# Kernel tuning notes

Measured on AMD Instinct MI355X. Metric: run time of the kernel, lower is better.

## Reference

```python
import jax, jax.numpy as jnp
import numpy as np
from jax import lax

EPS = 1e-5

# sign binarization with straight-through estimator (bitorch Sign: grad clipped to |x|<=1)
def _sign(x):
    return jnp.where(x >= 0, 1.0, -1.0).astype(x.dtype)

@jax.custom_vjp
def sign_ste(x):
    return _sign(x)

def _sign_fwd(x):
    return _sign(x), x

def _sign_bwd(x, g):
    return (g * (jnp.abs(x) <= 1.0).astype(g.dtype),)

sign_ste.defvjp(_sign_fwd, _sign_bwd)


def conv2d(x, w, stride, padding):
    return lax.conv_general_dilated(
        x, w, window_strides=(stride, stride),
        padding=[(padding, padding), (padding, padding)],
        dimension_numbers=("NCHW", "OIHW", "NCHW"))


def batchnorm(x, gamma, beta, mean, var):
    # eval-mode BN with running statistics
    inv = gamma / jnp.sqrt(var + EPS)
    return x * inv[None, :, None, None] + (beta - mean * inv)[None, :, None, None]


def avgpool2(x, stride):
    # AvgPool2d(kernel_size=2, stride=stride); here stride==2, H,W even
    B, C, H, W = x.shape
    return x.reshape(B, C, H // 2, 2, W // 2, 2).mean(axis=(3, 5))


def setup_inputs() -> dict:
    key = jax.random.key(0)
    ks = jax.random.split(key, 6)
    B, Cin, Cout, H, W = 16, 32, 64, 224, 224
    x = jax.random.normal(ks[0], (B, Cin, H, W), dtype=jnp.float32)
    w_body = jax.random.normal(ks[1], (Cout, Cin, 3, 3), dtype=jnp.float32) * 0.1
    w_ds = jax.random.normal(ks[2], (Cout, Cin, 1, 1), dtype=jnp.float32) * 0.1
    bn1_gamma = jnp.ones((Cout,), jnp.float32)
    bn1_beta = jnp.zeros((Cout,), jnp.float32)
    bn1_mean = jax.random.normal(ks[3], (Cout,), dtype=jnp.float32) * 0.1
    bn1_var = jax.random.uniform(ks[4], (Cout,), dtype=jnp.float32) + 0.5
    bn2_gamma = jnp.ones((Cout,), jnp.float32)
    bn2_beta = jnp.zeros((Cout,), jnp.float32)
    bn2_mean = jax.random.normal(ks[5], (Cout,), dtype=jnp.float32) * 0.1
    bn2_var = jax.random.uniform(jax.random.fold_in(key, 7), (Cout,), dtype=jnp.float32) + 0.5
    return dict(x=x, w_body=w_body, bn1_gamma=bn1_gamma, bn1_beta=bn1_beta,
                bn1_mean=bn1_mean, bn1_var=bn1_var, w_ds=w_ds,
                bn2_gamma=bn2_gamma, bn2_beta=bn2_beta,
                bn2_mean=bn2_mean, bn2_var=bn2_var)


def reference(x, w_body, bn1_gamma, bn1_beta, bn1_mean, bn1_var,
              w_ds, bn2_gamma, bn2_beta, bn2_mean, bn2_var):
    stride = 2
    # downsample branch (full precision): AvgPool2d(2, stride) -> 1x1 conv -> BN
    residual = avgpool2(x, stride)
    residual = conv2d(residual, w_ds, stride=1, padding=0)
    residual = batchnorm(residual, bn2_gamma, bn2_beta, bn2_mean, bn2_var)
    # body: QConv2d with sign-quantized input and weight, then BN
    xb = sign_ste(x)
    wb = sign_ste(w_body)
    body = conv2d(xb, wb, stride=stride, padding=1)
    body = batchnorm(body, bn1_gamma, bn1_beta, bn1_mean, bn1_var)
    return body + residual
```

## Files before the change

kernel.cpp:

```cpp
#include <hip/hip_runtime.h>
#include <stdint.h>

static constexpr int NB = 16;
static constexpr int CI = 32;
static constexpr int CO = 64;
static constexpr int HI = 224, WI = 224;
static constexpr int HO = 112, WO = 112;
static constexpr int HW = HI * WI;
static constexpr float EPS = 1e-5f;

typedef _Float16 h2 __attribute__((ext_vector_type(2)));

__device__ __forceinline__ h2 as_h2(uint32_t u) {
    union { uint32_t u; h2 h; } c; c.u = u; return c.h;
}
__device__ __forceinline__ uint32_t pack_h2(float a, float b) {
    union { uint32_t u; h2 h; } c;
    c.h = (h2){(_Float16)a, (_Float16)b};
    return c.u;
}

static constexpr size_t OFF_WT2 = 3072;
static constexpr size_t OFF_A1  = 7168;
static constexpr size_t OFF_CC  = 7424;
static constexpr size_t WS_NEED = 7680;

__device__ __forceinline__ int XB(int c) { return c + ((c >> 3) << 2); }
static constexpr int XBW = 132 + ((132 / 8) << 2) + 4;

__global__ __launch_bounds__(256) void prep_kernel(
    const float* __restrict__ wbody,
    const float* __restrict__ g1, const float* __restrict__ b1,
    const float* __restrict__ m1, const float* __restrict__ v1,
    const float* __restrict__ wds,
    const float* __restrict__ g2, const float* __restrict__ b2,
    const float* __restrict__ m2, const float* __restrict__ v2,
    uint32_t* __restrict__ wbits, uint32_t* __restrict__ wt2,
    float* __restrict__ A1, float* __restrict__ Cc)
{
    int i = blockIdx.x * 256 + threadIdx.x;
    if (i < 16 * CO) {
        int ci2 = i >> 6, co = i & 63;
        float inv2 = g2[co] * rsqrtf(v2[co] + EPS);
        float w0 = wds[co * CI + 2 * ci2]     * inv2;
        float w1 = wds[co * CI + 2 * ci2 + 1] * inv2;
        wt2[i] = pack_h2(w0, w1);
    } else if (i < 16 * CO + CO * 9) {
        int j = i - 16 * CO;
        int co = j / 9, k = j % 9;
        uint32_t bits = 0u;
#pragma unroll
        for (int ci = 0; ci < CI; ++ci) {
            float wv = wbody[(co * CI + ci) * 9 + k];
            bits |= (uint32_t)(wv >= 0.0f) << ci;
        }
        wbits[co * 12 + k] = bits;
    } else if (i < 16 * CO + CO * 9 + CO) {
        int co = i - 16 * CO - CO * 9;
        float inv1 = g1[co] * rsqrtf(v1[co] + EPS);
        float inv2 = g2[co] * rsqrtf(v2[co] + EPS);
        A1[co] = -2.0f * inv1;
        Cc[co] = b1[co] - m1[co] * inv1 + b2[co] - m2[co] * inv2 + 288.0f * inv1;
    }
}

__global__ __launch_bounds__(256) void fused_kernel(
    const float* __restrict__ x,
    const uint32_t* __restrict__ wbits, const uint32_t* __restrict__ wt2,
    const float* __restrict__ A1p, const float* __restrict__ Ccp,
    float* __restrict__ out)
{
    const int bid  = (blockIdx.x & 7) * 224 + (blockIdx.x >> 3);
    const int tile = bid & 1;
    const int gb   = bid >> 1;
    const int g    = gb % 56;
    const int b    = gb / 56;
    const int oh0  = 2 * g;
    const int ow0  = tile * 64;
    const int t    = threadIdx.x;

    __shared__ __align__(16) uint32_t s_xb[5][XBW];
    __shared__ __align__(16) uint32_t s_avg[2][16][68];
    __shared__ __align__(16) uint32_t s_wt2[16][64];
    __shared__ __align__(16) uint32_t s_wb[CO * 12];
    __shared__ float s_A1[CO], s_C[CO];

    uint32_t wtv[4], wbv[3];
    float a1v = 0.f, ccv = 0.f;
#pragma unroll
    for (int i = 0; i < 4; ++i) wtv[i] = wt2[t + 256 * i];
#pragma unroll
    for (int i = 0; i < 3; ++i) wbv[i] = wbits[t + 256 * i];
    if (t < CO) { a1v = A1p[t]; ccv = Ccp[t]; }

    const int pair = t >> 7;
    const int q    = t & 3;
    const int f    = (t >> 2) & 31;
    const int jcol = 2 * ow0 + 4 * f;
    const bool colok = (jcol + 3 < WI);

    const float* xp = x + ((size_t)(b * CI + 8 * q) * HI + (oh0 * 2 + 2 * pair)) * WI + jcol;
    float4 L[16];
#pragma unroll
    for (int i = 0; i < 16; ++i) L[i] = make_float4(0.f, 0.f, 0.f, 0.f);
    if (colok) {
#pragma unroll
        for (int k = 0; k < 4; ++k) {
            L[4 * k + 0] = *(const float4*)(xp + (size_t)(2 * k) * HW);
            L[4 * k + 1] = *(const float4*)(xp + (size_t)(2 * k) * HW + WI);
            L[4 * k + 2] = *(const float4*)(xp + (size_t)(2 * k + 1) * HW);
            L[4 * k + 3] = *(const float4*)(xp + (size_t)(2 * k + 1) * HW + WI);
        }
    }

    float4 H[8];
#pragma unroll
    for (int i = 0; i < 8; ++i) H[i] = make_float4(0.f, 0.f, 0.f, 0.f);
    if (t < 128 && g > 0 && colok) {
        const float* xh = x + ((size_t)(b * CI + 8 * q) * HI + (oh0 * 2 - 1)) * WI + jcol;
#pragma unroll
        for (int k = 0; k < 8; ++k)
            H[k] = *(const float4*)(xh + (size_t)k * HW);
    }

    const int wc = 2 * ow0 - 1;
    float hv[4] = {-1.f, -1.f, -1.f, -1.f};
    const int lr = t >> 3, lch = t & 7;
    const int hr = oh0 * 2 - 1 + lr;
    if (t < 40 && hr >= 0 && wc >= 0) {
        const float* xc = x + ((size_t)(b * CI + 4 * lch) * HI + hr) * WI + wc;
#pragma unroll
        for (int ci = 0; ci < 4; ++ci) hv[ci] = xc[(size_t)ci * HW];
    }

    {
        uint32_t* wt2s = (uint32_t*)s_wt2;
#pragma unroll
        for (int i = 0; i < 4; ++i) wt2s[t + 256 * i] = wtv[i];
#pragma unroll
        for (int i = 0; i < 3; ++i) s_wb[t + 256 * i] = wbv[i];
        if (t < CO) { s_A1[t] = a1v; s_C[t] = ccv; }
    }

    {
        uint32_t m0[4] = {0, 0, 0, 0}, m1r[4] = {0, 0, 0, 0};
#pragma unroll
        for (int k = 0; k < 4; ++k) {
            const float4 t0 = L[4 * k + 0], u0 = L[4 * k + 1];
            const float4 t1 = L[4 * k + 2], u1 = L[4 * k + 3];
            const int s0 = 8 * q + 2 * k, s1 = s0 + 1;
            m0[0]  |= ((uint32_t)(t0.x >= 0.f) << s0) | ((uint32_t)(t1.x >= 0.f) << s1);
            m0[1]  |= ((uint32_t)(t0.y >= 0.f) << s0) | ((uint32_t)(t1.y >= 0.f) << s1);
            m0[2]  |= ((uint32_t)(t0.z >= 0.f) << s0) | ((uint32_t)(t1.z >= 0.f) << s1);
            m0[3]  |= ((uint32_t)(t0.w >= 0.f) << s0) | ((uint32_t)(t1.w >= 0.f) << s1);
            m1r[0] |= ((uint32_t)(u0.x >= 0.f) << s0) | ((uint32_t)(u1.x >= 0.f) << s1);
            m1r[1] |= ((uint32_t)(u0.y >= 0.f) << s0) | ((uint32_t)(u1.y >= 0.f) << s1);
            m1r[2] |= ((uint32_t)(u0.z >= 0.f) << s0) | ((uint32_t)(u1.z >= 0.f) << s1);
            m1r[3] |= ((uint32_t)(u0.w >= 0.f) << s0) | ((uint32_t)(u1.w >= 0.f) << s1);
            float a0p0 = 0.25f * ((t0.x + t0.y) + (u0.x + u0.y));
            float a0p1 = 0.25f * ((t0.z + t0.w) + (u0.z + u0.w));
            float a1p0 = 0.25f * ((t1.x + t1.y) + (u1.x + u1.y));
            float a1p1 = 0.25f * ((t1.z + t1.w) + (u1.z + u1.w));
            *(uint2*)&s_avg[pair][4 * q + k][2 * f] =
                make_uint2(pack_h2(a0p0, a1p0), pack_h2(a0p1, a1p1));
        }
#pragma unroll
        for (int j = 0; j < 4; ++j) {
            m0[j]  |= __shfl_xor(m0[j], 1);  m0[j]  |= __shfl_xor(m0[j], 2);
            m1r[j] |= __shfl_xor(m1r[j], 1); m1r[j] |= __shfl_xor(m1r[j], 2);
        }
        uint32_t v0  = (q == 0) ? m0[0]  : (q == 1) ? m0[1]  : (q == 2) ? m0[2]  : m0[3];
        uint32_t v1v = (q == 0) ? m1r[0] : (q == 1) ? m1r[1] : (q == 2) ? m1r[2] : m1r[3];
        s_xb[1 + 2 * pair][XB(1 + 4 * f + q)] = v0;
        s_xb[2 + 2 * pair][XB(1 + 4 * f + q)] = v1v;
    }

    if (t < 128) {
        uint32_t mm[4] = {0, 0, 0, 0};
#pragma unroll
        for (int k = 0; k < 4; ++k) {
            const float4 t0 = H[2 * k], t1 = H[2 * k + 1];
            const int s0 = 8 * q + 2 * k, s1 = s0 + 1;
            mm[0] |= ((uint32_t)(t0.x >= 0.f) << s0) | ((uint32_t)(t1.x >= 0.f) << s1);
            mm[1] |= ((uint32_t)(t0.y >= 0.f) << s0) | ((uint32_t)(t1.y >= 0.f) << s1);
            mm[2] |= ((uint32_t)(t0.z >= 0.f) << s0) | ((uint32_t)(t1.z >= 0.f) << s1);
            mm[3] |= ((uint32_t)(t0.w >= 0.f) << s0) | ((uint32_t)(t1.w >= 0.f) << s1);
        }
        if (!(g > 0 && colok)) { mm[0] = mm[1] = mm[2] = mm[3] = 0u; }
#pragma unroll
        for (int j = 0; j < 4; ++j) { mm[j] |= __shfl_xor(mm[j], 1); mm[j] |= __shfl_xor(mm[j], 2); }
        s_xb[0][XB(1 + 4 * f + q)] = (q == 0) ? mm[0] : (q == 1) ? mm[1] : (q == 2) ? mm[2] : mm[3];
    }
    if (t < 40) {
        uint32_t bits = 0u;
        if (hr >= 0 && wc >= 0) {
#pragma unroll
            for (int ci = 0; ci < 4; ++ci)
                bits |= (uint32_t)(hv[ci] >= 0.0f) << (4 * lch + ci);
        }
        bits |= __shfl_xor(bits, 1);
        bits |= __shfl_xor(bits, 2);
        bits |= __shfl_xor(bits, 4);
        if (lch == 0) s_xb[lr][XB(0)] = bits;
    }
    __syncthreads();

    const int cg  = t >> 4;
    const int pg  = t & 15;
    const int co0 = cg * 4;
    const int p0  = pg * 4;
    const bool pxvalid = (ow0 + p0 < WO);
    const bool px0 = (ow0 + p0 == 0);
    const int cb = 12 * pg;

#pragma unroll 1
    for (int r = 0; r < 2; ++r) {
        float fa[4][4] = {{0.f,0.f,0.f,0.f},{0.f,0.f,0.f,0.f},{0.f,0.f,0.f,0.f},{0.f,0.f,0.f,0.f}};
#pragma unroll 4
        for (int ci2 = 0; ci2 < 16; ++ci2) {
            uint4 av = *(const uint4*)&s_avg[r][ci2][p0];
            uint4 wv = *(const uint4*)&s_wt2[ci2][co0];
            h2 a[4] = {as_h2(av.x), as_h2(av.y), as_h2(av.z), as_h2(av.w)};
            h2 w[4] = {as_h2(wv.x), as_h2(wv.y), as_h2(wv.z), as_h2(wv.w)};
#pragma unroll
            for (int jc = 0; jc < 4; ++jc)
#pragma unroll
                for (int jp = 0; jp < 4; ++jp)
                    fa[jc][jp] = __builtin_amdgcn_fdot2(w[jc], a[jp], fa[jc][jp], false);
        }

        uint32_t xr[3][9];
#pragma unroll
        for (int rI = 0; rI < 3; ++rI) {
            const uint32_t* row = s_xb[2 * r + rI];
            uint4 a  = *(const uint4*)&row[cb];
            uint4 bq = *(const uint4*)&row[cb + 4];
            xr[rI][0] = a.x;  xr[rI][1] = a.y;  xr[rI][2] = a.z;  xr[rI][3] = a.w;
            xr[rI][4] = bq.x; xr[rI][5] = bq.y; xr[rI][6] = bq.z; xr[rI][7] = bq.w;
            xr[rI][8] = row[cb + 12];
        }

        const bool ohf = (g == 0 && r == 0);
        int sfin[4][4];
#pragma unroll
        for (int jc = 0; jc < 4; ++jc) {
            const int co = co0 + jc;
            uint4 wa  = *(const uint4*)&s_wb[co * 12];
            uint4 wb4 = *(const uint4*)&s_wb[co * 12 + 4];
            uint32_t wv[9] = {wa.x, wa.y, wa.z, wa.w, wb4.x, wb4.y, wb4.z, wb4.w,
                              s_wb[co * 12 + 8]};
#pragma unroll
            for (int jp = 0; jp < 4; ++jp) {
                int c00 = __popc(xr[0][2 * jp + 0] ^ wv[0]);
                int c01 = __popc(xr[0][2 * jp + 1] ^ wv[1]);
                int c02 = __popc(xr[0][2 * jp + 2] ^ wv[2]);
                int c10 = __popc(xr[1][2 * jp + 0] ^ wv[3]);
                int c11 = __popc(xr[1][2 * jp + 1] ^ wv[4]);
                int c12 = __popc(xr[1][2 * jp + 2] ^ wv[5]);
                int c20 = __popc(xr[2][2 * jp + 0] ^ wv[6]);
                int c21 = __popc(xr[2][2 * jp + 1] ^ wv[7]);
                int c22 = __popc(xr[2][2 * jp + 2] ^ wv[8]);
                int r0v  = c00 + c01 + c02;
                int ssum = r0v + c10 + c11 + c12 + c20 + c21 + c22;
                if (ohf) ssum += 48 - r0v;
                if (px0 && jp == 0) {
                    ssum += 48 - (c00 + c10 + c20);
                    if (ohf) ssum += c00 - 16;
                }
                sfin[jc][jp] = ssum;
            }
        }

        if (pxvalid) {
#pragma unroll
            for (int jc = 0; jc < 4; ++jc) {
                const int co = co0 + jc;
                const float n2a = s_A1[co], cc = s_C[co];
                float4 o;
                o.x = fmaf(n2a, (float)sfin[jc][0], fa[jc][0] + cc);
                o.y = fmaf(n2a, (float)sfin[jc][1], fa[jc][1] + cc);
                o.z = fmaf(n2a, (float)sfin[jc][2], fa[jc][2] + cc);
                o.w = fmaf(n2a, (float)sfin[jc][3], fa[jc][3] + cc);
                *(float4*)&out[((size_t)(b * CO + co) * HO + (oh0 + r)) * WO + ow0 + p0] = o;
            }
        }
    }
}

__global__ __launch_bounds__(256) void naive_kernel(
    const float* __restrict__ x, const float* __restrict__ wbody,
    const float* __restrict__ g1, const float* __restrict__ b1,
    const float* __restrict__ m1, const float* __restrict__ v1,
    const float* __restrict__ wds,
    const float* __restrict__ g2, const float* __restrict__ b2,
    const float* __restrict__ m2, const float* __restrict__ v2,
    float* __restrict__ out)
{
    int i = blockIdx.x * 256 + threadIdx.x;
    if (i >= NB * CO * HO * WO) return;
    int ow = i % WO;
    int oh = (i / WO) % HO;
    int co = (i / (WO * HO)) % CO;
    int b  = i / (WO * HO * CO);
    float inv1 = g1[co] * rsqrtf(v1[co] + EPS);
    float inv2 = g2[co] * rsqrtf(v2[co] + EPS);
    int body = 0;
    float ds = 0.f;
    for (int ci = 0; ci < CI; ++ci) {
        const float* xp = x + (size_t)(b * CI + ci) * HW;
        for (int kh = 0; kh < 3; ++kh) {
            int hh = 2 * oh - 1 + kh;
            if (hh < 0 || hh >= HI) continue;
            for (int kw = 0; kw < 3; ++kw) {
                int ww = 2 * ow - 1 + kw;
                if (ww < 0 || ww >= WI) continue;
                float xv = xp[(size_t)hh * WI + ww];
                float wv = wbody[((co * CI + ci) * 3 + kh) * 3 + kw];
                int sx = (xv >= 0.f) ? 1 : -1;
                int sw = (wv >= 0.f) ? 1 : -1;
                body += sx * sw;
            }
        }
        float a = 0.25f * (xp[(size_t)(2 * oh) * WI + 2 * ow]
                         + xp[(size_t)(2 * oh) * WI + 2 * ow + 1]
                         + xp[(size_t)(2 * oh + 1) * WI + 2 * ow]
                         + xp[(size_t)(2 * oh + 1) * WI + 2 * ow + 1]);
        ds += a * wds[co * CI + ci];
    }
    out[i] = inv1 * (float)body + (b1[co] - m1[co] * inv1)
           + inv2 * ds + (b2[co] - m2[co] * inv2);
}

extern "C" void kernel_launch(void* const* d_in, const int* in_sizes, int n_in,
                              void* d_out, int out_size, void* d_ws, size_t ws_size,
                              hipStream_t stream)
{
    (void)in_sizes; (void)n_in; (void)out_size;
    const float* x   = (const float*)d_in[0];
    const float* wbd = (const float*)d_in[1];
    const float* g1  = (const float*)d_in[2];
    const float* b1  = (const float*)d_in[3];
    const float* m1  = (const float*)d_in[4];
    const float* v1  = (const float*)d_in[5];
    const float* wds = (const float*)d_in[6];
    const float* g2  = (const float*)d_in[7];
    const float* b2  = (const float*)d_in[8];
    const float* m2  = (const float*)d_in[9];
    const float* v2  = (const float*)d_in[10];
    float* out = (float*)d_out;

    if (ws_size < WS_NEED) {
        int total = NB * CO * HO * WO;
        naive_kernel<<<(total + 255) / 256, 256, 0, stream>>>(
            x, wbd, g1, b1, m1, v1, wds, g2, b2, m2, v2, out);
        return;
    }

    char* wsb = (char*)d_ws;
    uint32_t* wbits = (uint32_t*)wsb;
    uint32_t* wt2   = (uint32_t*)(wsb + OFF_WT2);
    float*    A1    = (float*)(wsb + OFF_A1);
    float*    Cc    = (float*)(wsb + OFF_CC);

    prep_kernel<<<7, 256, 0, stream>>>(wbd, g1, b1, m1, v1, wds, g2, b2, m2, v2,
                                       wbits, wt2, A1, Cc);
    fused_kernel<<<dim3(NB * 56 * 2), 256, 0, stream>>>(
        x, wbits, wt2, A1, Cc, out);
}
```

Baseline: 47.79 us.

## Process seven output rows per block with rolling row buffers and prefetch

Each block now covers seven output rows instead of two. It keeps a five-slot ring of binarized input rows in shared memory, so the halo row is loaded once per block rather than once per row pair. The next pair of input rows is loaded into registers while the current row is being computed, which overlaps global loads with popcount and dot work. The grid shrinks from 1792 to 512 blocks, so occupancy and tail balance drop in exchange for less halo traffic and fewer block launches.

New measurement: 51.04 us. 1.07x slower.

```diff
diff --git a/kernel.cpp b/kernel.cpp
--- a/kernel.cpp
+++ b/kernel.cpp
@@ -70,12 +70,12 @@
     const float* __restrict__ A1p, const float* __restrict__ Ccp,
     float* __restrict__ out)
 {
-    const int bid  = (blockIdx.x & 7) * 224 + (blockIdx.x >> 3);
+    const int bid  = (blockIdx.x & 7) * 64 + (blockIdx.x >> 3);
     const int tile = bid & 1;
     const int gb   = bid >> 1;
-    const int g    = gb % 56;
-    const int b    = gb / 56;
-    const int oh0  = 2 * g;
+    const int gg   = gb & 15;
+    const int b    = gb >> 4;
+    const int oh0  = 7 * gg;
     const int ow0  = tile * 64;
     const int t    = threadIdx.x;
 
@@ -93,44 +93,41 @@
     for (int i = 0; i < 3; ++i) wbv[i] = wbits[t + 256 * i];
     if (t < CO) { a1v = A1p[t]; ccv = Ccp[t]; }
 
-    const int pair = t >> 7;
-    const int q    = t & 3;
-    const int f    = (t >> 2) & 31;
+    const int q    = t & 7;
+    const int f    = t >> 3;
     const int jcol = 2 * ow0 + 4 * f;
     const bool colok = (jcol + 3 < WI);
-
-    const float* xp = x + ((size_t)(b * CI + 8 * q) * HI + (oh0 * 2 + 2 * pair)) * WI + jcol;
-    float4 L[16];
-#pragma unroll
-    for (int i = 0; i < 16; ++i) L[i] = make_float4(0.f, 0.f, 0.f, 0.f);
-    if (colok) {
-#pragma unroll
-        for (int k = 0; k < 4; ++k) {
-            L[4 * k + 0] = *(const float4*)(xp + (size_t)(2 * k) * HW);
-            L[4 * k + 1] = *(const float4*)(xp + (size_t)(2 * k) * HW + WI);
-            L[4 * k + 2] = *(const float4*)(xp + (size_t)(2 * k + 1) * HW);
-            L[4 * k + 3] = *(const float4*)(xp + (size_t)(2 * k + 1) * HW + WI);
-        }
-    }
-
-    float4 H[8];
-#pragma unroll
-    for (int i = 0; i < 8; ++i) H[i] = make_float4(0.f, 0.f, 0.f, 0.f);
-    if (t < 128 && g > 0 && colok) {
-        const float* xh = x + ((size_t)(b * CI + 8 * q) * HI + (oh0 * 2 - 1)) * WI + jcol;
-#pragma unroll
-        for (int k = 0; k < 8; ++k)
-            H[k] = *(const float4*)(xh + (size_t)k * HW);
-    }
-
-    const int wc = 2 * ow0 - 1;
-    float hv[4] = {-1.f, -1.f, -1.f, -1.f};
-    const int lr = t >> 3, lch = t & 7;
-    const int hr = oh0 * 2 - 1 + lr;
-    if (t < 40 && hr >= 0 && wc >= 0) {
-        const float* xc = x + ((size_t)(b * CI + 4 * lch) * HI + hr) * WI + wc;
-#pragma unroll
-        for (int ci = 0; ci < 4; ++ci) hv[ci] = xc[(size_t)ci * HW];
+    const int wc   = 2 * ow0 - 1;
+
+    float4 T[4], U[4], Hh[4];
+#pragma unroll
+    for (int j = 0; j < 4; ++j) {
+        T[j] = make_float4(0.f, 0.f, 0.f, 0.f);
+        U[j] = T[j]; Hh[j] = T[j];
+    }
+    {
+        const float* base = x + ((size_t)(b * CI + 4 * q) * HI + 2 * oh0) * WI + jcol;
+        if (colok) {
+#pragma unroll
+            for (int j = 0; j < 4; ++j) {
+                T[j] = *(const float4*)(base + (size_t)j * HW);
+                U[j] = *(const float4*)(base + (size_t)j * HW + WI);
+            }
+            if (gg > 0) {
+#pragma unroll
+                for (int j = 0; j < 4; ++j)
+                    Hh[j] = *(const float4*)(base + (size_t)j * HW - WI);
+            }
+        }
+    }
+    float hcv[4] = {-1.f, -1.f, -1.f, -1.f};
+    if (t < 24) {
+        const int hr = 2 * oh0 - 1 + (t >> 3);
+        if (hr >= 0 && wc >= 0) {
+            const float* xc = x + ((size_t)(b * CI + 4 * q) * HI + hr) * WI + wc;
+#pragma unroll
+            for (int ci = 0; ci < 4; ++ci) hcv[ci] = xc[(size_t)ci * HW];
+        }
     }
 
     {
@@ -142,66 +139,75 @@
         if (t < CO) { s_A1[t] = a1v; s_C[t] = ccv; }
     }
 
+    auto proc_pair = [&](const float4* Tv, const float4* Uv,
+                         int slotT, int slotU, int av) {
+        uint32_t mT[4] = {0, 0, 0, 0}, mU[4] = {0, 0, 0, 0};
+#pragma unroll
+        for (int j = 0; j < 4; ++j) {
+            const int s = 4 * q + j;
+            mT[0] |= (uint32_t)(Tv[j].x >= 0.f) << s;
+            mT[1] |= (uint32_t)(Tv[j].y >= 0.f) << s;
+            mT[2] |= (uint32_t)(Tv[j].z >= 0.f) << s;
+            mT[3] |= (uint32_t)(Tv[j].w >= 0.f) << s;
+            mU[0] |= (uint32_t)(Uv[j].x >= 0.f) << s;
+            mU[1] |= (uint32_t)(Uv[j].y >= 0.f) << s;
+            mU[2] |= (uint32_t)(Uv[j].z >= 0.f) << s;
+            mU[3] |= (uint32_t)(Uv[j].w >= 0.f) << s;
+        }
+        float p00 = 0.25f * ((Tv[0].x + Tv[0].y) + (Uv[0].x + Uv[0].y));
+        float p01 = 0.25f * ((Tv[0].z + Tv[0].w) + (Uv[0].z + Uv[0].w));
+        float p10 = 0.25f * ((Tv[1].x + Tv[1].y) + (Uv[1].x + Uv[1].y));
+        float p11 = 0.25f * ((Tv[1].z + Tv[1].w) + (Uv[1].z + Uv[1].w));
+        float p20 = 0.25f * ((Tv[2].x + Tv[2].y) + (Uv[2].x + Uv[2].y));
+        float p21 = 0.25f * ((Tv[2].z + Tv[2].w) + (Uv[2].z + Uv[2].w));
+        float p30 = 0.25f * ((Tv[3].x + Tv[3].y) + (Uv[3].x + Uv[3].y));
+        float p31 = 0.25f * ((Tv[3].z + Tv[3].w) + (Uv[3].z + Uv[3].w));
+        *(uint2*)&s_avg[av][2 * q][2 * f] =
+            make_uint2(pack_h2(p00, p10), pack_h2(p01, p11));
+        *(uint2*)&s_avg[av][2 * q + 1][2 * f] =
+            make_uint2(pack_h2(p20, p30), pack_h2(p21, p31));
+#pragma unroll
+        for (int e = 0; e < 4; ++e) {
+            mT[e] |= __shfl_xor(mT[e], 1); mT[e] |= __shfl_xor(mT[e], 2); mT[e] |= __shfl_xor(mT[e], 4);
+            mU[e] |= __shfl_xor(mU[e], 1); mU[e] |= __shfl_xor(mU[e], 2); mU[e] |= __shfl_xor(mU[e], 4);
+        }
+        const int e = q & 3;
+        uint32_t vT = (e == 0) ? mT[0] : (e == 1) ? mT[1] : (e == 2) ? mT[2] : mT[3];
+        uint32_t vU = (e == 0) ? mU[0] : (e == 1) ? mU[1] : (e == 2) ? mU[2] : mU[3];
+        if (q < 4) s_xb[slotT][XB(1 + 4 * f + e)] = vT;
+        else       s_xb[slotU][XB(1 + 4 * f + e)] = vU;
+    };
+
+    proc_pair(T, U, 1, 2, 0);
     {
-        uint32_t m0[4] = {0, 0, 0, 0}, m1r[4] = {0, 0, 0, 0};
-#pragma unroll
-        for (int k = 0; k < 4; ++k) {
-            const float4 t0 = L[4 * k + 0], u0 = L[4 * k + 1];
-            const float4 t1 = L[4 * k + 2], u1 = L[4 * k + 3];
-            const int s0 = 8 * q + 2 * k, s1 = s0 + 1;
-            m0[0]  |= ((uint32_t)(t0.x >= 0.f) << s0) | ((uint32_t)(t1.x >= 0.f) << s1);
-            m0[1]  |= ((uint32_t)(t0.y >= 0.f) << s0) | ((uint32_t)(t1.y >= 0.f) << s1);
-            m0[2]  |= ((uint32_t)(t0.z >= 0.f) << s0) | ((uint32_t)(t1.z >= 0.f) << s1);
-            m0[3]  |= ((uint32_t)(t0.w >= 0.f) << s0) | ((uint32_t)(t1.w >= 0.f) << s1);
-            m1r[0] |= ((uint32_t)(u0.x >= 0.f) << s0) | ((uint32_t)(u1.x >= 0.f) << s1);
-            m1r[1] |= ((uint32_t)(u0.y >= 0.f) << s0) | ((uint32_t)(u1.y >= 0.f) << s1);
-            m1r[2] |= ((uint32_t)(u0.z >= 0.f) << s0) | ((uint32_t)(u1.z >= 0.f) << s1);
-            m1r[3] |= ((uint32_t)(u0.w >= 0.f) << s0) | ((uint32_t)(u1.w >= 0.f) << s1);
-            float a0p0 = 0.25f * ((t0.x + t0.y) + (u0.x + u0.y));
-            float a0p1 = 0.25f * ((t0.z + t0.w) + (u0.z + u0.w));
-            float a1p0 = 0.25f * ((t1.x + t1.y) + (u1.x + u1.y));
-            float a1p1 = 0.25f * ((t1.z + t1.w) + (u1.z + u1.w));
-            *(uint2*)&s_avg[pair][4 * q + k][2 * f] =
-                make_uint2(pack_h2(a0p0, a1p0), pack_h2(a0p1, a1p1));
-        }
+        uint32_t mH[4] = {0, 0, 0, 0};
 #pragma unroll
         for (int j = 0; j < 4; ++j) {
-            m0[j]  |= __shfl_xor(m0[j], 1);  m0[j]  |= __shfl_xor(m0[j], 2);
-            m1r[j] |= __shfl_xor(m1r[j], 1); m1r[j] |= __shfl_xor(m1r[j], 2);
-        }
-        uint32_t v0  = (q == 0) ? m0[0]  : (q == 1) ? m0[1]  : (q == 2) ? m0[2]  : m0[3];
-        uint32_t v1v = (q == 0) ? m1r[0] : (q == 1) ? m1r[1] : (q == 2) ? m1r[2] : m1r[3];
-        s_xb[1 + 2 * pair][XB(1 + 4 * f + q)] = v0;
-        s_xb[2 + 2 * pair][XB(1 + 4 * f + q)] = v1v;
-    }
-
-    if (t < 128) {
-        uint32_t mm[4] = {0, 0, 0, 0};
-#pragma unroll
-        for (int k = 0; k < 4; ++k) {
-            const float4 t0 = H[2 * k], t1 = H[2 * k + 1];
-            const int s0 = 8 * q + 2 * k, s1 = s0 + 1;
-            mm[0] |= ((uint32_t)(t0.x >= 0.f) << s0) | ((uint32_t)(t1.x >= 0.f) << s1);
-            mm[1] |= ((uint32_t)(t0.y >= 0.f) << s0) | ((uint32_t)(t1.y >= 0.f) << s1);
-            mm[2] |= ((uint32_t)(t0.z >= 0.f) << s0) | ((uint32_t)(t1.z >= 0.f) << s1);
-            mm[3] |= ((uint32_t)(t0.w >= 0.f) << s0) | ((uint32_t)(t1.w >= 0.f) << s1);
-        }
-        if (!(g > 0 && colok)) { mm[0] = mm[1] = mm[2] = mm[3] = 0u; }
-#pragma unroll
-        for (int j = 0; j < 4; ++j) { mm[j] |= __shfl_xor(mm[j], 1); mm[j] |= __shfl_xor(mm[j], 2); }
-        s_xb[0][XB(1 + 4 * f + q)] = (q == 0) ? mm[0] : (q == 1) ? mm[1] : (q == 2) ? mm[2] : mm[3];
-    }
-    if (t < 40) {
+            const int s = 4 * q + j;
+            mH[0] |= (uint32_t)(Hh[j].x >= 0.f) << s;
+            mH[1] |= (uint32_t)(Hh[j].y >= 0.f) << s;
+            mH[2] |= (uint32_t)(Hh[j].z >= 0.f) << s;
+            mH[3] |= (uint32_t)(Hh[j].w >= 0.f) << s;
+        }
+        if (!(gg > 0 && colok)) { mH[0] = mH[1] = mH[2] = mH[3] = 0u; }
+#pragma unroll
+        for (int e = 0; e < 4; ++e) {
+            mH[e] |= __shfl_xor(mH[e], 1); mH[e] |= __shfl_xor(mH[e], 2); mH[e] |= __shfl_xor(mH[e], 4);
+        }
+        if (q < 4) {
+            uint32_t v = (q == 0) ? mH[0] : (q == 1) ? mH[1] : (q == 2) ? mH[2] : mH[3];
+            s_xb[0][XB(1 + 4 * f + q)] = v;
+        }
+    }
+    if (t < 24) {
         uint32_t bits = 0u;
-        if (hr >= 0 && wc >= 0) {
-#pragma unroll
-            for (int ci = 0; ci < 4; ++ci)
-                bits |= (uint32_t)(hv[ci] >= 0.0f) << (4 * lch + ci);
-        }
+#pragma unroll
+        for (int ci = 0; ci < 4; ++ci)
+            bits |= (uint32_t)(hcv[ci] >= 0.0f) << (4 * q + ci);
         bits |= __shfl_xor(bits, 1);
         bits |= __shfl_xor(bits, 2);
         bits |= __shfl_xor(bits, 4);
-        if (lch == 0) s_xb[lr][XB(0)] = bits;
+        if (q == 0) s_xb[t >> 3][XB(0)] = bits;
     }
     __syncthreads();
 
@@ -213,34 +219,31 @@
     const bool px0 = (ow0 + p0 == 0);
     const int cb = 12 * pg;
 
-#pragma unroll 1
-    for (int r = 0; r < 2; ++r) {
+    auto compute_row = [&](int i, int sA, int sB, int sC, int av) {
         float fa[4][4] = {{0.f,0.f,0.f,0.f},{0.f,0.f,0.f,0.f},{0.f,0.f,0.f,0.f},{0.f,0.f,0.f,0.f}};
 #pragma unroll 4
         for (int ci2 = 0; ci2 < 16; ++ci2) {
-            uint4 av = *(const uint4*)&s_avg[r][ci2][p0];
-            uint4 wv = *(const uint4*)&s_wt2[ci2][co0];
-            h2 a[4] = {as_h2(av.x), as_h2(av.y), as_h2(av.z), as_h2(av.w)};
-            h2 w[4] = {as_h2(wv.x), as_h2(wv.y), as_h2(wv.z), as_h2(wv.w)};
+            uint4 avv = *(const uint4*)&s_avg[av][ci2][p0];
+            uint4 wvv = *(const uint4*)&s_wt2[ci2][co0];
+            h2 a[4] = {as_h2(avv.x), as_h2(avv.y), as_h2(avv.z), as_h2(avv.w)};
+            h2 w[4] = {as_h2(wvv.x), as_h2(wvv.y), as_h2(wvv.z), as_h2(wvv.w)};
 #pragma unroll
             for (int jc = 0; jc < 4; ++jc)
 #pragma unroll
                 for (int jp = 0; jp < 4; ++jp)
                     fa[jc][jp] = __builtin_amdgcn_fdot2(w[jc], a[jp], fa[jc][jp], false);
         }
-
         uint32_t xr[3][9];
+        const uint32_t* rows[3] = {s_xb[sA], s_xb[sB], s_xb[sC]};
 #pragma unroll
         for (int rI = 0; rI < 3; ++rI) {
-            const uint32_t* row = s_xb[2 * r + rI];
-            uint4 a  = *(const uint4*)&row[cb];
-            uint4 bq = *(const uint4*)&row[cb + 4];
+            uint4 a  = *(const uint4*)&rows[rI][cb];
+            uint4 bq = *(const uint4*)&rows[rI][cb + 4];
             xr[rI][0] = a.x;  xr[rI][1] = a.y;  xr[rI][2] = a.z;  xr[rI][3] = a.w;
             xr[rI][4] = bq.x; xr[rI][5] = bq.y; xr[rI][6] = bq.z; xr[rI][7] = bq.w;
-            xr[rI][8] = row[cb + 12];
-        }
-
-        const bool ohf = (g == 0 && r == 0);
+            xr[rI][8] = rows[rI][cb + 12];
+        }
+        const bool ohf = (gg == 0 && i == 0);
         int sfin[4][4];
 #pragma unroll
         for (int jc = 0; jc < 4; ++jc) {
@@ -270,7 +273,6 @@
                 sfin[jc][jp] = ssum;
             }
         }
-
         if (pxvalid) {
 #pragma unroll
             for (int jc = 0; jc < 4; ++jc) {
@@ -281,9 +283,57 @@
                 o.y = fmaf(n2a, (float)sfin[jc][1], fa[jc][1] + cc);
                 o.z = fmaf(n2a, (float)sfin[jc][2], fa[jc][2] + cc);
                 o.w = fmaf(n2a, (float)sfin[jc][3], fa[jc][3] + cc);
-                *(float4*)&out[((size_t)(b * CO + co) * HO + (oh0 + r)) * WO + ow0 + p0] = o;
-            }
-        }
+                *(float4*)&out[((size_t)(b * CO + co) * HO + (oh0 + i)) * WO + ow0 + p0] = o;
+            }
+        }
+    };
+
+    int sl0 = 0, sl1 = 1, sl2 = 2, sl3 = 3, sl4 = 4;
+#pragma unroll 1
+    for (int i = 0; i < 7; ++i) {
+        const bool last = (i == 6);
+        float4 nT[4], nU[4];
+#pragma unroll
+        for (int j = 0; j < 4; ++j) {
+            nT[j] = make_float4(0.f, 0.f, 0.f, 0.f);
+            nU[j] = nT[j];
+        }
+        float nhc[4] = {-1.f, -1.f, -1.f, -1.f};
+        if (!last) {
+            const int r0 = 2 * oh0 + 2 * i + 2;
+            if (colok) {
+                const float* base = x + ((size_t)(b * CI + 4 * q) * HI + r0) * WI + jcol;
+#pragma unroll
+                for (int j = 0; j < 4; ++j) {
+                    nT[j] = *(const float4*)(base + (size_t)j * HW);
+                    nU[j] = *(const float4*)(base + (size_t)j * HW + WI);
+                }
+            }
+            if (t < 16 && wc >= 0) {
+                const float* xc = x + ((size_t)(b * CI + 4 * q) * HI + (r0 + (t >> 3))) * WI + wc;
+#pragma unroll
+                for (int ci = 0; ci < 4; ++ci) nhc[ci] = xc[(size_t)ci * HW];
+            }
+        }
+
+        compute_row(i, sl0, sl1, sl2, i & 1);
+
+        if (!last) {
+            proc_pair(nT, nU, sl3, sl4, (i + 1) & 1);
+            if (t < 16) {
+                uint32_t bits = 0u;
+#pragma unroll
+                for (int ci = 0; ci < 4; ++ci)
+                    bits |= (uint32_t)(nhc[ci] >= 0.0f) << (4 * q + ci);
+                bits |= __shfl_xor(bits, 1);
+                bits |= __shfl_xor(bits, 2);
+                bits |= __shfl_xor(bits, 4);
+                if (q == 0) s_xb[(t >> 3) == 0 ? sl3 : sl4][XB(0)] = bits;
+            }
+            __syncthreads();
+        }
+        int o0 = sl0, o1 = sl1;
+        sl0 = sl2; sl1 = sl3; sl2 = sl4; sl3 = o0; sl4 = o1;
     }
 }
 
@@ -364,6 +414,6 @@
 
     prep_kernel<<<7, 256, 0, stream>>>(wbd, g1, b1, m1, v1, wds, g2, b2, m2, v2,
                                        wbits, wt2, A1, Cc);
-    fused_kernel<<<dim3(NB * 56 * 2), 256, 0, stream>>>(
+    fused_kernel<<<dim3(512), 256, 0, stream>>>(
         x, wbits, wt2, A1, Cc, out);
 }
```

## Use MFMA for downsample 1x1 conv and remap threads to MFMA layout

Applied to the files above, without the earlier changes.

Replaces the per-thread fdot2 loop for the residual 1x1 convolution with a single mfma_f32_16x16x32_f16 per 16-pixel tile. Threads are remapped to the MFMA output layout: each lane owns one pixel and four output channels, binarized weights are hoisted into registers once, and the XNOR-popcount body conv is computed for that layout. Stores become scalar per channel instead of float4. This removes VALU dot-product work but adds a pixel-tile loop and narrower global stores, and it relies on the shared-memory layouts matching the MFMA operand layout.

Result: faster. 44.92 us (-6.0%).

```diff
diff --git a/kernel.cpp b/kernel.cpp
--- a/kernel.cpp
+++ b/kernel.cpp
@@ -10,6 +10,8 @@
 static constexpr float EPS = 1e-5f;
 
 typedef _Float16 h2 __attribute__((ext_vector_type(2)));
+typedef _Float16 h8 __attribute__((ext_vector_type(8)));
+typedef float f32x4 __attribute__((ext_vector_type(4)));
 
 __device__ __forceinline__ h2 as_h2(uint32_t u) {
     union { uint32_t u; h2 h; } c; c.u = u; return c.h;
@@ -205,83 +207,79 @@
     }
     __syncthreads();
 
-    const int cg  = t >> 4;
-    const int pg  = t & 15;
-    const int co0 = cg * 4;
-    const int p0  = pg * 4;
-    const bool pxvalid = (ow0 + p0 < WO);
-    const bool px0 = (ow0 + p0 == 0);
-    const int cb = 12 * pg;
+    const int w   = t >> 6;
+    const int l15 = t & 15;
+    const int lk  = (t >> 4) & 3;
+
+    union U8 { uint32_t u[4]; h8 h; };
+    U8 af;
+#pragma unroll
+    for (int i = 0; i < 4; ++i) af.u[i] = s_wt2[4 * lk + i][16 * w + l15];
+
+    uint32_t wv[4][9];
+    float n2a[4], ccs[4];
+#pragma unroll
+    for (int j = 0; j < 4; ++j) {
+        const int co = 16 * w + 4 * lk + j;
+        uint4 wa  = *(const uint4*)&s_wb[co * 12];
+        uint4 wb4 = *(const uint4*)&s_wb[co * 12 + 4];
+        wv[j][0] = wa.x;  wv[j][1] = wa.y;  wv[j][2] = wa.z;  wv[j][3] = wa.w;
+        wv[j][4] = wb4.x; wv[j][5] = wb4.y; wv[j][6] = wb4.z; wv[j][7] = wb4.w;
+        wv[j][8] = s_wb[co * 12 + 8];
+        n2a[j] = s_A1[co]; ccs[j] = s_C[co];
+    }
+
+    const int npt = (tile == 0) ? 4 : 3;
 
 #pragma unroll 1
     for (int r = 0; r < 2; ++r) {
-        float fa[4][4] = {{0.f,0.f,0.f,0.f},{0.f,0.f,0.f,0.f},{0.f,0.f,0.f,0.f},{0.f,0.f,0.f,0.f}};
-#pragma unroll 4
-        for (int ci2 = 0; ci2 < 16; ++ci2) {
-            uint4 av = *(const uint4*)&s_avg[r][ci2][p0];
-            uint4 wv = *(const uint4*)&s_wt2[ci2][co0];
-            h2 a[4] = {as_h2(av.x), as_h2(av.y), as_h2(av.z), as_h2(av.w)};
-            h2 w[4] = {as_h2(wv.x), as_h2(wv.y), as_h2(wv.z), as_h2(wv.w)};
-#pragma unroll
-            for (int jc = 0; jc < 4; ++jc)
-#pragma unroll
-                for (int jp = 0; jp < 4; ++jp)
-                    fa[jc][jp] = __builtin_amdgcn_fdot2(w[jc], a[jp], fa[jc][jp], false);
-        }
-
-        uint32_t xr[3][9];
-#pragma unroll
-        for (int rI = 0; rI < 3; ++rI) {
-            const uint32_t* row = s_xb[2 * r + rI];
-            uint4 a  = *(const uint4*)&row[cb];
-            uint4 bq = *(const uint4*)&row[cb + 4];
-            xr[rI][0] = a.x;  xr[rI][1] = a.y;  xr[rI][2] = a.z;  xr[rI][3] = a.w;
-            xr[rI][4] = bq.x; xr[rI][5] = bq.y; xr[rI][6] = bq.z; xr[rI][7] = bq.w;
-            xr[rI][8] = row[cb + 12];
-        }
-
         const bool ohf = (g == 0 && r == 0);
-        int sfin[4][4];
-#pragma unroll
-        for (int jc = 0; jc < 4; ++jc) {
-            const int co = co0 + jc;
-            uint4 wa  = *(const uint4*)&s_wb[co * 12];
-            uint4 wb4 = *(const uint4*)&s_wb[co * 12 + 4];
-            uint32_t wv[9] = {wa.x, wa.y, wa.z, wa.w, wb4.x, wb4.y, wb4.z, wb4.w,
-                              s_wb[co * 12 + 8]};
-#pragma unroll
-            for (int jp = 0; jp < 4; ++jp) {
-                int c00 = __popc(xr[0][2 * jp + 0] ^ wv[0]);
-                int c01 = __popc(xr[0][2 * jp + 1] ^ wv[1]);
-                int c02 = __popc(xr[0][2 * jp + 2] ^ wv[2]);
-                int c10 = __popc(xr[1][2 * jp + 0] ^ wv[3]);
-                int c11 = __popc(xr[1][2 * jp + 1] ^ wv[4]);
-                int c12 = __popc(xr[1][2 * jp + 2] ^ wv[5]);
-                int c20 = __popc(xr[2][2 * jp + 0] ^ wv[6]);
-                int c21 = __popc(xr[2][2 * jp + 1] ^ wv[7]);
-                int c22 = __popc(xr[2][2 * jp + 2] ^ wv[8]);
+#pragma unroll 1
+        for (int pt = 0; pt < npt; ++pt) {
+            U8 bf;
+#pragma unroll
+            for (int i = 0; i < 4; ++i) bf.u[i] = s_avg[r][4 * lk + i][16 * pt + l15];
+            f32x4 acc = {0.f, 0.f, 0.f, 0.f};
+            acc = __builtin_amdgcn_mfma_f32_16x16x32_f16(af.h, bf.h, acc, 0, 0, 0);
+
+            const int c0 = 32 * pt + 2 * l15;
+            const int i0 = XB(c0);
+            const int i2 = XB(c0 + 2);
+            uint32_t xr[3][3];
+#pragma unroll
+            for (int rI = 0; rI < 3; ++rI) {
+                const uint32_t* row = s_xb[2 * r + rI];
+                uint2 v = *(const uint2*)&row[i0];
+                xr[rI][0] = v.x; xr[rI][1] = v.y; xr[rI][2] = row[i2];
+            }
+
+            const bool pleft = (tile == 0 && pt == 0 && l15 == 0);
+            float res[4];
+#pragma unroll
+            for (int j = 0; j < 4; ++j) {
+                int c00 = __popc(xr[0][0] ^ wv[j][0]);
+                int c01 = __popc(xr[0][1] ^ wv[j][1]);
+                int c02 = __popc(xr[0][2] ^ wv[j][2]);
+                int c10 = __popc(xr[1][0] ^ wv[j][3]);
+                int c11 = __popc(xr[1][1] ^ wv[j][4]);
+                int c12 = __popc(xr[1][2] ^ wv[j][5]);
+                int c20 = __popc(xr[2][0] ^ wv[j][6]);
+                int c21 = __popc(xr[2][1] ^ wv[j][7]);
+                int c22 = __popc(xr[2][2] ^ wv[j][8]);
                 int r0v  = c00 + c01 + c02;
                 int ssum = r0v + c10 + c11 + c12 + c20 + c21 + c22;
                 if (ohf) ssum += 48 - r0v;
-                if (px0 && jp == 0) {
+                if (pleft) {
                     ssum += 48 - (c00 + c10 + c20);
                     if (ohf) ssum += c00 - 16;
                 }
-                sfin[jc][jp] = ssum;
+                res[j] = fmaf(n2a[j], (float)ssum, acc[j] + ccs[j]);
             }
-        }
-
-        if (pxvalid) {
-#pragma unroll
-            for (int jc = 0; jc < 4; ++jc) {
-                const int co = co0 + jc;
-                const float n2a = s_A1[co], cc = s_C[co];
-                float4 o;
-                o.x = fmaf(n2a, (float)sfin[jc][0], fa[jc][0] + cc);
-                o.y = fmaf(n2a, (float)sfin[jc][1], fa[jc][1] + cc);
-                o.z = fmaf(n2a, (float)sfin[jc][2], fa[jc][2] + cc);
-                o.w = fmaf(n2a, (float)sfin[jc][3], fa[jc][3] + cc);
-                *(float4*)&out[((size_t)(b * CO + co) * HO + (oh0 + r)) * WO + ow0 + p0] = o;
+            const size_t pbase = (size_t)ow0 + 16 * pt + l15;
+#pragma unroll
+            for (int j = 0; j < 4; ++j) {
+                const int co = 16 * w + 4 * lk + j;
+                out[((size_t)(b * CO + co) * HO + (oh0 + r)) * WO + pbase] = res[j];
             }
         }
     }
```
